# Performance work log

Measured on AMD Instinct MI355X. Metric: run time of the kernel, lower is better.

## Reference

```python
import jax, jax.numpy as jnp
import numpy as np

N = 100000
E = 1000000
IN_DIM = 64
OUT_DIM = 64


def setup_inputs() -> dict:
    key = jax.random.key(0)
    k1, k2, k3, k4 = jax.random.split(key, 4)
    x = jax.random.normal(k1, (N, IN_DIM), dtype=jnp.float32)
    edge_index = jax.random.randint(k2, (2, E), 0, N, dtype=jnp.int64)
    # nn.Linear(in_dim, out_dim): weight (out,in), bias (out,)
    bound = 1.0 / np.sqrt(IN_DIM)
    W = jax.random.uniform(k3, (OUT_DIM, IN_DIM), dtype=jnp.float32, minval=-bound, maxval=bound)
    b = jax.random.uniform(k4, (OUT_DIM,), dtype=jnp.float32, minval=-bound, maxval=bound)
    return {"x": x, "edge_index": edge_index, "W": W, "b": b}


def reference(x, edge_index, W, b):
    i = edge_index[0]  # target nodes (E,)
    j = edge_index[1]  # source nodes (E,)
    msg = x[j] @ W.T + b  # (E, out_dim)
    n = x.shape[0]
    out = jax.ops.segment_sum(msg, i, num_segments=n)  # (N, out_dim)
    deg = jax.ops.segment_sum(jnp.ones((i.shape[0],), dtype=msg.dtype), i, num_segments=n)
    deg = jnp.maximum(deg, 1.0)[:, None]
    return out / deg
```

## Files before the change

### kernel.cpp

```cpp
#include <hip/hip_runtime.h>

constexpr int N_NODES = 100000;
constexpr int N_EDGES = 1000000;
constexpr int DIM = 64;

constexpr int BNODES = 256;
constexpr int NBUCK  = (N_NODES + BNODES - 1) / BNODES;
constexpr int SCAP   = 3584;
constexpr int CHUNK  = 8192;
constexpr int NWG_A  = (N_EDGES + CHUNK - 1) / CHUNK;

constexpr int CAP  = 16;
constexpr int MAXO = 32768;

constexpr int TILE = 64;
constexpr int PAD  = 65;

__global__ __launch_bounds__(256) void bin_edges(
    const int* __restrict__ eidx, int* __restrict__ gcur,
    int* __restrict__ staging)
{
    __shared__ int            sval[CHUNK];
    __shared__ unsigned short sbkt[CHUNK];
    __shared__ int hist[512];
    __shared__ int base[512];
    __shared__ int gbase[512];
    __shared__ int ps[256];

    const int tid = threadIdx.x;
    const int e0  = blockIdx.x * CHUNK;
    const int n   = (N_EDGES - e0 < CHUNK) ? (N_EDGES - e0) : CHUNK;

    for (int t = tid; t < 512; t += 256) hist[t] = 0;
    __syncthreads();

    for (int t = tid; t < n; t += 256) {
        int i = eidx[e0 + t];
        atomicAdd(&hist[i >> 8], 1);
    }
    __syncthreads();

    int h0 = hist[2 * tid], h1 = hist[2 * tid + 1];
    int pv = h0 + h1;
    ps[tid] = pv;
    __syncthreads();
    for (int d = 1; d < 256; d <<= 1) {
        int t = (tid >= d) ? ps[tid - d] : 0;
        __syncthreads();
        ps[tid] += t;
        __syncthreads();
    }
    int pex = ps[tid] - pv;
    base[2 * tid]     = pex;
    base[2 * tid + 1] = pex + h0;
    hist[2 * tid]     = pex;
    hist[2 * tid + 1] = pex + h0;
    __syncthreads();

    for (int t = tid; t < n; t += 256) {
        int i  = eidx[e0 + t];
        int j  = eidx[N_EDGES + e0 + t];
        int bk = i >> 8;
        int pos = atomicAdd(&hist[bk], 1);
        sval[pos] = ((i & 255) << 17) | j;
        sbkt[pos] = (unsigned short)bk;
    }
    __syncthreads();

    for (int t = tid; t < 512; t += 256) {
        int c = hist[t] - base[t];
        gbase[t] = (c > 0) ? atomicAdd(&gcur[t], c) : 0;
    }
    __syncthreads();

    for (int t = tid; t < n; t += 256) {
        int bk = sbkt[t];
        int dst = gbase[bk] + (t - base[bk]);
        if (dst < SCAP)
            staging[bk * SCAP + dst] = sval[t];
    }
}

__global__ __launch_bounds__(256) void fused_gather_mm(
    const float* __restrict__ x, const int* __restrict__ gcur,
    const int* __restrict__ staging,
    const float* __restrict__ W, const float* __restrict__ b,
    int* __restrict__ noflow, int* __restrict__ oflow,
    int* __restrict__ deg_g, float* __restrict__ out)
{
    __shared__ float tile[TILE * PAD];
    __shared__ int   lds_slot[TILE * CAP];
    __shared__ int   lcnt[TILE];

    const int tid  = threadIdx.x;
    const int base = blockIdx.x * TILE;
    const int bk   = blockIdx.x >> 2;
    const int sub  = blockIdx.x & 3;

    if (tid < TILE) lcnt[tid] = 0;
    __syncthreads();

    int m = gcur[bk];
    if (m > SCAP) m = SCAP;
    const int sg = bk * SCAP;
    for (int t = tid; t < m; t += 256) {
        int pk  = staging[sg + t];
        int off = pk >> 17;
        if ((off >> 6) == sub) {
            int r = off & 63;
            int pos = atomicAdd(&lcnt[r], 1);
            if (pos < CAP) {
                lds_slot[(r << 4) + pos] = pk & 0x1FFFF;
            } else {
                int o = atomicAdd(noflow, 1);
                if (o < MAXO) {
                    oflow[2 * o]     = (bk << 8) + off;
                    oflow[2 * o + 1] = pk & 0x1FFFF;
                }
            }
        }
    }
    __syncthreads();

    if (tid < TILE) {
        int g = base + tid;
        if (g < N_NODES) deg_g[g] = lcnt[tid];
    }

    const int lane = tid & 63;
    const int wid  = tid >> 6;
    const int grp  = lane >> 4;
    const int l16  = lane & 15;
    const int c4   = l16 << 2;

#pragma unroll
    for (int pack = 0; pack < 4; ++pack) {
        const int row    = wid * 16 + pack * 4 + grp;
        const int node   = base + row;
        const bool valid = (node < N_NODES);
        const int d_true = valid ? lcnt[row] : 0;
        const int d      = (d_true < CAP) ? d_true : CAP;

        const int jrow = lds_slot[(row << 4) + l16];

        float sx = 0.0f, sy = 0.0f, sz = 0.0f, sw = 0.0f;
#pragma unroll
        for (int u = 0; u < CAP; ++u) {
            const int  ju = __shfl(jrow, (grp << 4) | u);
            const bool ok = (u < d);
            const int  jj = ok ? ju : 0;
            const float4 v = *reinterpret_cast<const float4*>(
                x + ((size_t)jj << 6) + c4);
            sx += ok ? v.x : 0.0f;
            sy += ok ? v.y : 0.0f;
            sz += ok ? v.z : 0.0f;
            sw += ok ? v.w : 0.0f;
        }

        const float inv = (d_true > 0) ? 1.0f / (float)d_true : 0.0f;
        const int tb = row * PAD + c4;
        tile[tb + 0] = sx * inv;
        tile[tb + 1] = sy * inv;
        tile[tb + 2] = sz * inv;
        tile[tb + 3] = sw * inv;
    }
    __syncthreads();

    const int nd  = tid & 63;
    const int d0u = __builtin_amdgcn_readfirstlane((tid >> 6) << 4);
    const float* __restrict__ Wr = W + (size_t)d0u * DIM;

    float acc[16];
#pragma unroll
    for (int q = 0; q < 16; ++q) acc[q] = 0.0f;

#pragma unroll 4
    for (int k = 0; k < DIM; ++k) {
        float a = tile[nd * PAD + k];
#pragma unroll
        for (int q = 0; q < 16; ++q)
            acc[q] = fmaf(a, Wr[(size_t)q * DIM + k], acc[q]);
    }

    const int dg = lcnt[nd];
    __syncthreads();
#pragma unroll
    for (int q = 0; q < 16; ++q) {
        float v = (dg > 0) ? (acc[q] + b[d0u + q]) : 0.0f;
        tile[nd * PAD + d0u + q] = v;
    }
    __syncthreads();

#pragma unroll
    for (int r = 0; r < 16; ++r) {
        int idx = r * 256 + tid;
        int row = idx >> 6, d = idx & 63;
        int g = base + row;
        if (g < N_NODES)
            out[(size_t)g * DIM + d] = tile[row * PAD + d];
    }
}

__global__ __launch_bounds__(256) void fixup_overflow(
    const int* __restrict__ noflow, const int* __restrict__ oflow,
    const int* __restrict__ deg_g, const float* __restrict__ x,
    const float* __restrict__ W, float* __restrict__ out)
{
    int m = *noflow;
    if (m > MAXO) m = MAXO;
    const int lane = threadIdx.x & 63;
    const int wv   = (blockIdx.x * 256 + threadIdx.x) >> 6;
    const int nwv  = (gridDim.x * 256) >> 6;
    const float* __restrict__ wr = W + ((size_t)lane << 6);
    for (int o = wv; o < m; o += nwv) {
        const int i = oflow[2 * o];
        const int j = oflow[2 * o + 1];
        const float inv = 1.0f / (float)deg_g[i];
        const float* __restrict__ xr = x + ((size_t)j << 6);
        float acc = 0.0f;
#pragma unroll
        for (int k4 = 0; k4 < 16; ++k4) {
            const float4 xv  = *reinterpret_cast<const float4*>(xr + 4 * k4);
            const float4 wv4 = *reinterpret_cast<const float4*>(wr + 4 * k4);
            acc = fmaf(xv.x, wv4.x, acc);
            acc = fmaf(xv.y, wv4.y, acc);
            acc = fmaf(xv.z, wv4.z, acc);
            acc = fmaf(xv.w, wv4.w, acc);
        }
        atomicAdd(&out[((size_t)i << 6) + lane], acc * inv);
    }
}

extern "C" void kernel_launch(void* const* d_in, const int* in_sizes, int n_in,
                              void* d_out, int out_size, void* d_ws, size_t ws_size,
                              hipStream_t stream) {
    const float* x  = (const float*)d_in[0];
    const int*   ei = (const int*)d_in[1];
    const float* W  = (const float*)d_in[2];
    const float* b  = (const float*)d_in[3];
    float* out = (float*)d_out;

    int* gcur    = (int*)d_ws;
    int* noflow  = gcur + NBUCK;
    int* oflow   = noflow + 1;
    int* deg_g   = oflow + 2 * MAXO;
    int* staging = deg_g + N_NODES;

    hipMemsetAsync(gcur, 0, (NBUCK + 1) * sizeof(int), stream);

    bin_edges<<<NWG_A, 256, 0, stream>>>(ei, gcur, staging);
    fused_gather_mm<<<(N_NODES + TILE - 1) / TILE, 256, 0, stream>>>(
        x, gcur, staging, W, b, noflow, oflow, deg_g, out);
    fixup_overflow<<<128, 256, 0, stream>>>(noflow, oflow, deg_g, x, W, out);
}
```

Before: 210.0 us.

## Simplify edge binning to direct global scatter and batch gather loads

The binning kernel drops the LDS counting-sort staging and prefix scan. Each block now reserves global space per bucket right after the histogram and scatters packed edges straight to staging through per-bucket LDS counters, with chunk size reduced to 2048 so more blocks run. The gather loop reads all 16 neighbor indices from LDS up front and issues all 16 float4 loads before reducing, which raises memory-level parallelism at the cost of more registers. Global staging writes become less coalesced, and the node-validity check on degree is removed, relying on lcnt being zero for out-of-range rows.

```diff
diff --git a/kernel.cpp b/kernel.cpp
--- a/kernel.cpp
+++ b/kernel.cpp
@@ -7,7 +7,7 @@
 constexpr int BNODES = 256;
 constexpr int NBUCK  = (N_NODES + BNODES - 1) / BNODES;
 constexpr int SCAP   = 3584;
-constexpr int CHUNK  = 8192;
+constexpr int CHUNK  = 2048;
 constexpr int NWG_A  = (N_EDGES + CHUNK - 1) / CHUNK;
 
 constexpr int CAP  = 16;
@@ -20,18 +20,15 @@
     const int* __restrict__ eidx, int* __restrict__ gcur,
     int* __restrict__ staging)
 {
-    __shared__ int            sval[CHUNK];
-    __shared__ unsigned short sbkt[CHUNK];
-    __shared__ int hist[512];
-    __shared__ int base[512];
-    __shared__ int gbase[512];
-    __shared__ int ps[256];
+    __shared__ int hist[NBUCK];
+    __shared__ int gbase[NBUCK];
+    __shared__ int cur[NBUCK];
 
     const int tid = threadIdx.x;
     const int e0  = blockIdx.x * CHUNK;
     const int n   = (N_EDGES - e0 < CHUNK) ? (N_EDGES - e0) : CHUNK;
 
-    for (int t = tid; t < 512; t += 256) hist[t] = 0;
+    for (int t = tid; t < NBUCK; t += 256) hist[t] = 0;
     __syncthreads();
 
     for (int t = tid; t < n; t += 256) {
@@ -40,44 +37,21 @@
     }
     __syncthreads();
 
-    int h0 = hist[2 * tid], h1 = hist[2 * tid + 1];
-    int pv = h0 + h1;
-    ps[tid] = pv;
-    __syncthreads();
-    for (int d = 1; d < 256; d <<= 1) {
-        int t = (tid >= d) ? ps[tid - d] : 0;
-        __syncthreads();
-        ps[tid] += t;
-        __syncthreads();
-    }
-    int pex = ps[tid] - pv;
-    base[2 * tid]     = pex;
-    base[2 * tid + 1] = pex + h0;
-    hist[2 * tid]     = pex;
-    hist[2 * tid + 1] = pex + h0;
+    for (int t = tid; t < NBUCK; t += 256) {
+        int c = hist[t];
+        gbase[t] = (c > 0) ? atomicAdd(&gcur[t], c) : 0;
+        cur[t] = 0;
+    }
     __syncthreads();
 
     for (int t = tid; t < n; t += 256) {
         int i  = eidx[e0 + t];
         int j  = eidx[N_EDGES + e0 + t];
         int bk = i >> 8;
-        int pos = atomicAdd(&hist[bk], 1);
-        sval[pos] = ((i & 255) << 17) | j;
-        sbkt[pos] = (unsigned short)bk;
-    }
-    __syncthreads();
-
-    for (int t = tid; t < 512; t += 256) {
-        int c = hist[t] - base[t];
-        gbase[t] = (c > 0) ? atomicAdd(&gcur[t], c) : 0;
-    }
-    __syncthreads();
-
-    for (int t = tid; t < n; t += 256) {
-        int bk = sbkt[t];
-        int dst = gbase[bk] + (t - base[bk]);
+        int pos = atomicAdd(&cur[bk], 1);
+        int dst = gbase[bk] + pos;
         if (dst < SCAP)
-            staging[bk * SCAP + dst] = sval[t];
+            staging[bk * SCAP + dst] = ((i & 255) << 17) | j;
     }
 }
 
@@ -136,25 +110,28 @@
 #pragma unroll
     for (int pack = 0; pack < 4; ++pack) {
         const int row    = wid * 16 + pack * 4 + grp;
-        const int node   = base + row;
-        const bool valid = (node < N_NODES);
-        const int d_true = valid ? lcnt[row] : 0;
+        const int d_true = lcnt[row];
         const int d      = (d_true < CAP) ? d_true : CAP;
 
-        const int jrow = lds_slot[(row << 4) + l16];
+        int jv[16];
+#pragma unroll
+        for (int u = 0; u < 16; ++u) jv[u] = lds_slot[(row << 4) + u];
+
+        float4 vb[16];
+#pragma unroll
+        for (int u = 0; u < 16; ++u) {
+            const int jj = (u < d) ? jv[u] : 0;
+            vb[u] = *reinterpret_cast<const float4*>(x + ((size_t)jj << 6) + c4);
+        }
 
         float sx = 0.0f, sy = 0.0f, sz = 0.0f, sw = 0.0f;
 #pragma unroll
-        for (int u = 0; u < CAP; ++u) {
-            const int  ju = __shfl(jrow, (grp << 4) | u);
+        for (int u = 0; u < 16; ++u) {
             const bool ok = (u < d);
-            const int  jj = ok ? ju : 0;
-            const float4 v = *reinterpret_cast<const float4*>(
-                x + ((size_t)jj << 6) + c4);
-            sx += ok ? v.x : 0.0f;
-            sy += ok ? v.y : 0.0f;
-            sz += ok ? v.z : 0.0f;
-            sw += ok ? v.w : 0.0f;
+            sx += ok ? vb[u].x : 0.0f;
+            sy += ok ? vb[u].y : 0.0f;
+            sz += ok ? vb[u].z : 0.0f;
+            sw += ok ? vb[u].w : 0.0f;
         }
 
         const float inv = (d_true > 0) ? 1.0f / (float)d_true : 0.0f;
```

After: 200.9 us. -4.3%, faster.
